# Kernel tuning notes

Measured on AMD Instinct MI355X. Metric: run time of the kernel, lower is better.

The kernel has to match this reference:

```python
import jax, jax.numpy as jnp
import numpy as np
import math

V, D, H, F, L, S, B = 50257, 1024, 16, 4096, 4, 2048, 2
DK = D // H

def setup_inputs() -> dict:
    key = jax.random.key(0)
    ks = iter(jax.random.split(key, 32))
    std = 0.02
    def nrm(shape):
        return (std * jax.random.normal(next(ks), shape)).astype(jnp.float32)
    inp = {
        "x": jax.random.randint(next(ks), (B, S), 0, V, dtype=jnp.int32),
        "emb": nrm((V, D)),
        "ln1_g": jnp.ones((L, D), jnp.float32), "ln1_b": jnp.zeros((L, D), jnp.float32),
        "wq": nrm((L, D, D)), "wk": nrm((L, D, D)), "wv": nrm((L, D, D)), "wo": nrm((L, D, D)),
        "ln2_g": jnp.ones((L, D), jnp.float32), "ln2_b": jnp.zeros((L, D), jnp.float32),
        "w1": nrm((L, D, F)), "b1": jnp.zeros((L, F), jnp.float32),
        "w2": nrm((L, F, D)), "b2": jnp.zeros((L, D), jnp.float32),
        "lnf_g": jnp.ones((D,), jnp.float32), "lnf_b": jnp.zeros((D,), jnp.float32),
        "head_w": nrm((D, V)), "head_b": jnp.zeros((V,), jnp.float32),
    }
    return inp

def _layernorm(x, g, b, eps=1e-5):
    mu = jnp.mean(x, axis=-1, keepdims=True)
    var = jnp.var(x, axis=-1, keepdims=True)
    return (x - mu) * jax.lax.rsqrt(var + eps) * g + b

def _posenc(seq_len, d_model, dtype):
    pos = jnp.arange(seq_len, dtype=jnp.float32)[:, None]                  # [S,1]
    div = jnp.exp(jnp.arange(0, d_model, 2, dtype=jnp.float32) * (-math.log(10000.0) / d_model))
    ang = pos * div                                                        # [S,D/2]
    pe = jnp.stack([jnp.sin(ang), jnp.cos(ang)], axis=-1).reshape(seq_len, d_model)
    return pe.astype(dtype)

def reference(x, emb, ln1_g, ln1_b, wq, wk, wv, wo, ln2_g, ln2_b, w1, b1, w2, b2, lnf_g, lnf_b, head_w, head_b):
    b, s = x.shape
    h = emb[x] + _posenc(s, D, emb.dtype)[None]                            # [B,S,D]
    causal = jnp.tril(jnp.ones((s, s), dtype=bool))                       # True = keep
    scale = 1.0 / math.sqrt(DK)
    neg_inf = jnp.finfo(h.dtype).min
    for l in range(L):
        # --- attention sublayer ---
        hn = _layernorm(h, ln1_g[l], ln1_b[l])
        q = (hn @ wq[l]).reshape(b, s, H, DK)
        k = (hn @ wk[l]).reshape(b, s, H, DK)
        v = (hn @ wv[l]).reshape(b, s, H, DK)
        scores = jnp.einsum("bqhd,bkhd->bhqk", q, k) * scale
        scores = jnp.where(causal[None, None], scores, neg_inf)
        w = jax.nn.softmax(scores, axis=-1)
        attn = jnp.einsum("bhqk,bkhd->bqhd", w, v).reshape(b, s, D)
        h = h + attn @ wo[l]
        # --- FFN sublayer ---
        hn = _layernorm(h, ln2_g[l], ln2_b[l])
        h = h + jax.nn.relu(hn @ w1[l] + b1[l]) @ w2[l] + b2[l]
    h = _layernorm(h, lnf_g, lnf_b)
    logits = h @ head_w + head_b                                           # [B,S,V]
    return logits
```

## Files before the change

### kernel.cpp

```cpp
#include <hip/hip_runtime.h>
#include <math.h>

#define VOCAB 50257
#define VPAD  50432
#define DM    1024
#define NH    16
#define DKH   64
#define FF    4096
#define NL    4
#define SEQ   2048
#define BATCH 2
#define MROWS (BATCH*SEQ)

typedef __bf16 bf16_t;
typedef __bf16 bf16x8 __attribute__((ext_vector_type(8)));
typedef __bf16 bf16x4 __attribute__((ext_vector_type(4)));
typedef float  f32x4  __attribute__((ext_vector_type(4)));

typedef void as1_void __attribute__((address_space(1)));
typedef void as3_void __attribute__((address_space(3)));

__device__ __forceinline__ void gload_lds16(const void* g, void* l) {
  __builtin_amdgcn_global_load_lds((as1_void*)g, (as3_void*)l, 16, 0, 0);
}

__device__ __forceinline__ uint32_t lds_addr32(const void* p) {
  return (uint32_t)(uintptr_t)(as3_void*)p;
}

__device__ __forceinline__ bf16x8 dsr128(uint32_t addr) {
  bf16x8 v;
  asm volatile("ds_read_b128 %0, %1" : "=v"(v) : "v"(addr));
  return v;
}

#define FENCE asm volatile("" ::: "memory")
#define BAR() do { FENCE; __builtin_amdgcn_s_barrier(); FENCE; } while (0)
#define LGKM0_FENCE() do { \
  asm volatile("s_waitcnt lgkmcnt(0)" ::: "memory"); \
  __builtin_amdgcn_sched_barrier(0); \
} while (0)

__global__ __launch_bounds__(256) void embed_kernel(const int* __restrict__ x,
    const float* __restrict__ emb, float* __restrict__ h) {
  int row = blockIdx.x;
  int s = row & (SEQ - 1);
  int d = threadIdx.x * 4;
  const float* e = emb + (size_t)x[row] * DM + d;
  float4 v = *(const float4*)e;
  float vin[4] = {v.x, v.y, v.z, v.w};
  float out[4];
#pragma unroll
  for (int j = 0; j < 4; ++j) {
    int dd = d + j;
    int i = dd >> 1;
    float freq = expf(-0.017988946039016376f * (float)i);
    float ang = (float)s * freq;
    float pe = (dd & 1) ? cosf(ang) : sinf(ang);
    out[j] = vin[j] + pe;
  }
  *(float4*)(h + (size_t)row * DM + d) = make_float4(out[0], out[1], out[2], out[3]);
}

__global__ __launch_bounds__(256) void ln_kernel(const float* __restrict__ x,
    const float* __restrict__ g, const float* __restrict__ b, bf16_t* __restrict__ out) {
  int row = blockIdx.x;
  int tid = threadIdx.x, lane = tid & 63, wave = tid >> 6;
  const float* xr = x + (size_t)row * DM;
  float4 v = ((const float4*)xr)[tid];
  float s1 = v.x + v.y + v.z + v.w;
  float s2 = v.x * v.x + v.y * v.y + v.z * v.z + v.w * v.w;
#pragma unroll
  for (int d = 1; d < 64; d <<= 1) { s1 += __shfl_xor(s1, d); s2 += __shfl_xor(s2, d); }
  __shared__ float red[8];
  if (lane == 0) { red[wave] = s1; red[4 + wave] = s2; }
  __syncthreads();
  s1 = red[0] + red[1] + red[2] + red[3];
  s2 = red[4] + red[5] + red[6] + red[7];
  float mu = s1 * (1.0f / DM);
  float var = s2 * (1.0f / DM) - mu * mu;
  float rs = rsqrtf(var + 1e-5f);
  float4 gv = ((const float4*)g)[tid];
  float4 bv = ((const float4*)b)[tid];
  bf16x4 o;
  o[0] = (bf16_t)((v.x - mu) * rs * gv.x + bv.x);
  o[1] = (bf16_t)((v.y - mu) * rs * gv.y + bv.y);
  o[2] = (bf16_t)((v.z - mu) * rs * gv.z + bv.z);
  o[3] = (bf16_t)((v.w - mu) * rs * gv.w + bv.w);
  *(bf16x4*)(out + (size_t)row * DM + tid * 4) = o;
}

__global__ __launch_bounds__(256) void transpose_cast_kernel(const float* __restrict__ in,
    bf16_t* __restrict__ out, int K, int N, int Npad) {
  __shared__ float tile[32][33];
  int n0 = blockIdx.x * 32, k0 = blockIdx.y * 32;
  int tx = threadIdx.x & 31, ty = threadIdx.x >> 5;
#pragma unroll
  for (int kk = ty; kk < 32; kk += 8) {
    int n = n0 + tx;
    tile[kk][tx] = (n < N) ? in[(size_t)(k0 + kk) * N + n] : 0.f;
  }
  __syncthreads();
#pragma unroll
  for (int nn = ty; nn < 32; nn += 8) {
    out[(size_t)(n0 + nn) * K + k0 + tx] = (bf16_t)tile[tx][nn];
  }
}

__global__ __launch_bounds__(256) void qkvtrans_kernel(const float* __restrict__ wq,
    const float* __restrict__ wk, const float* __restrict__ wv, bf16_t* __restrict__ out) {
  __shared__ float tile[32][33];
  int z = blockIdx.z;
  const float* in = (z == 0) ? wq : (z == 1) ? wk : wv;
  bf16_t* dst = out + (size_t)z * DM * DM;
  int n0 = blockIdx.x * 32, k0 = blockIdx.y * 32;
  int tx = threadIdx.x & 31, ty = threadIdx.x >> 5;
#pragma unroll
  for (int kk = ty; kk < 32; kk += 8)
    tile[kk][tx] = in[(size_t)(k0 + kk) * DM + n0 + tx];
  __syncthreads();
#pragma unroll
  for (int nn = ty; nn < 32; nn += 8)
    dst[(size_t)(n0 + nn) * DM + k0 + tx] = (bf16_t)tile[tx][nn];
}

__global__ __launch_bounds__(256) void vtrans_kernel(const bf16_t* __restrict__ qkv,
    bf16_t* __restrict__ vT) {
  int sb = blockIdx.x, hh = blockIdx.y, bb = blockIdx.z;
  __shared__ bf16_t t[64][72];
  int tid = threadIdx.x;
  const bf16_t* src = qkv + ((size_t)bb * SEQ + sb * 64) * (3 * DM) + 2 * DM + hh * DKH;
#pragma unroll
  for (int c = 0; c < 2; ++c) {
    int u = c * 256 + tid;
    int s = u >> 3, d8 = u & 7;
    *(bf16x8*)&t[s][d8 * 8] = *(const bf16x8*)(src + (size_t)s * (3 * DM) + d8 * 8);
  }
  __syncthreads();
  bf16_t* dst = vT + ((size_t)(bb * NH + hh) * DKH) * SEQ + sb * 64;
#pragma unroll
  for (int c = 0; c < 2; ++c) {
    int u = c * 256 + tid;
    int dk = u >> 3, s8 = u & 7;
    bf16x8 v;
#pragma unroll
    for (int j = 0; j < 8; ++j) v[j] = t[s8 * 8 + j][dk];
    *(bf16x8*)(dst + (size_t)dk * SEQ + s8 * 8) = v;
  }
}

__global__ __launch_bounds__(256, 2) void gemm128_kernel(
    const bf16_t* __restrict__ A, const bf16_t* __restrict__ Bt, int K,
    const float* __restrict__ bias, const float* __restrict__ Rsd,
    float* Cf, bf16_t* Cb, int ldc, int Nvalid, int relu, int gridM, int gridN) {
  __shared__ __align__(16) bf16_t lds[32768];

  int nwg = gridM * gridN;
  int orig = blockIdx.x;
  int q = nwg >> 3, rr = nwg & 7;
  int xcd = orig & 7, idx = orig >> 3;
  int swz = (xcd < rr ? xcd * (q + 1) : rr * (q + 1) + (xcd - rr) * q) + idx;
  int bm = swz % gridM, bn = swz / gridM;
  int m0 = bm * 128, n0 = bn * 128;

  int tid = threadIdx.x, lane = tid & 63, wave = tid >> 6;
  int g = lane >> 4, r = lane & 15;
  int wr = wave >> 1, wc = wave & 1;

  f32x4 zero = {0.f, 0.f, 0.f, 0.f};
  f32x4 acc[4][4];
#pragma unroll
  for (int i = 0; i < 4; ++i)
#pragma unroll
    for (int j = 0; j < 4; ++j) acc[i][j] = zero;

  const bf16_t* Abase = A + (size_t)m0 * K;
  const bf16_t* Bbase = Bt + (size_t)n0 * K;
  int NT = K >> 6;

  uint32_t L0 = lds_addr32(lds);
  uint32_t aF = L0 + (uint32_t)((g * 128 + wr * 64 + r) * 16);
  uint32_t bF = L0 + 32768u + (uint32_t)((g * 128 + wc * 64 + r) * 16);

  auto stage = [&](int t) {
    int b = t & 1, k0 = t << 6;
    bf16_t* dA = lds + (size_t)b * 8192;
    bf16_t* dB = lds + 16384 + (size_t)b * 8192;
#pragma unroll
    for (int j = 0; j < 4; ++j) {
      int u = j * 256 + tid;
      int row = u & 127, k8 = u >> 7;
      gload_lds16(Abase + (size_t)row * K + k0 + k8 * 8, dA + (j * 256 + wave * 64) * 8);
    }
#pragma unroll
    for (int j = 0; j < 4; ++j) {
      int u = j * 256 + tid;
      int row = u & 127, k8 = u >> 7;
      gload_lds16(Bbase + (size_t)row * K + k0 + k8 * 8, dB + (j * 256 + wave * 64) * 8);
    }
  };

  stage(0);
  if (NT > 1) {
    stage(1);
    asm volatile("s_waitcnt vmcnt(8)" ::: "memory");
  } else {
    asm volatile("s_waitcnt vmcnt(0)" ::: "memory");
  }
  BAR();

  for (int t = 0; t < NT; ++t) {
    uint32_t boff = (uint32_t)((t & 1) << 14);
    bf16x8 af[4][2], bfr[4][2];
#pragma unroll
    for (int mr = 0; mr < 4; ++mr)
#pragma unroll
      for (int kk = 0; kk < 2; ++kk)
        af[mr][kk] = dsr128(aF + boff + (uint32_t)(kk * 8192 + mr * 256));
#pragma unroll
    for (int nr = 0; nr < 4; ++nr)
#pragma unroll
      for (int kk = 0; kk < 2; ++kk)
        bfr[nr][kk] = dsr128(bF + boff + (uint32_t)(kk * 8192 + nr * 256));
    LGKM0_FENCE();
    BAR();
    if (t + 2 < NT) stage(t + 2);
    __builtin_amdgcn_s_setprio(1);
#pragma unroll
    for (int mr = 0; mr < 4; ++mr)
#pragma unroll
      for (int nr = 0; nr < 4; ++nr) {
        acc[mr][nr] = __builtin_amdgcn_mfma_f32_16x16x32_bf16(af[mr][0], bfr[nr][0], acc[mr][nr], 0, 0, 0);
        acc[mr][nr] = __builtin_amdgcn_mfma_f32_16x16x32_bf16(af[mr][1], bfr[nr][1], acc[mr][nr], 0, 0, 0);
      }
    __builtin_amdgcn_s_setprio(0);
    __builtin_amdgcn_sched_barrier(0);
    if (t + 2 < NT) {
      asm volatile("s_waitcnt vmcnt(8)" ::: "memory");
    } else {
      asm volatile("s_waitcnt vmcnt(0)" ::: "memory");
    }
    BAR();
  }

#pragma unroll
  for (int mr = 0; mr < 4; ++mr) {
    int row = m0 + wr * 64 + mr * 16 + g * 4;
#pragma unroll
    for (int nr = 0; nr < 4; ++nr) {
      int col = n0 + wc * 64 + nr * 16 + r;
      if (col < Nvalid) {
        float bval = bias ? bias[col] : 0.f;
#pragma unroll
        for (int i = 0; i < 4; ++i) {
          float vv = acc[mr][nr][i] + bval;
          if (relu) vv = fmaxf(vv, 0.f);
          size_t idxo = (size_t)(row + i) * ldc + col;
          if (Rsd) vv += Rsd[idxo];
          if (Cf) Cf[idxo] = vv;
          if (Cb) Cb[idxo] = (bf16_t)vv;
        }
      }
    }
  }
}

__global__ __launch_bounds__(512, 2) void gemm256_kernel(
    const bf16_t* __restrict__ A, const bf16_t* __restrict__ Bt, int K,
    const float* __restrict__ bias, float* Cf, bf16_t* Cb,
    int ldc, int Nvalid, int relu, int gridM, int gridN) {
  __shared__ __align__(16) bf16_t lds[65536];

  int nwg = gridM * gridN;
  int orig = blockIdx.x;
  int q = nwg >> 3, rr = nwg & 7;
  int xcd = orig & 7, idx = orig >> 3;
  int swz = (xcd < rr ? xcd * (q + 1) : rr * (q + 1) + (xcd - rr) * q) + idx;
  int bm = swz % gridM, bn = swz / gridM;
  int m0 = bm * 256, n0 = bn * 256;

  int tid = threadIdx.x, lane = tid & 63, wave = tid >> 6;
  int g = lane >> 4, r = lane & 15;
  int wr = wave >> 2, wc = wave & 3;

  f32x4 zero = {0.f, 0.f, 0.f, 0.f};
  f32x4 acc[8][4];
#pragma unroll
  for (int i = 0; i < 8; ++i)
#pragma unroll
    for (int j = 0; j < 4; ++j) acc[i][j] = zero;

  const bf16_t* Ab = A + (size_t)m0 * K;
  const bf16_t* Bb = Bt + (size_t)n0 * K;
  int NT = K >> 6;

  uint32_t L0 = lds_addr32(lds);
  uint32_t laneOff = (uint32_t)(g * 2048 + r * 16);
  uint32_t aBase0 = L0 + ((uint32_t)wr << 14) + laneOff;
  uint32_t bBase0 = L0 + 65536u + ((uint32_t)(wc >> 1) << 14) + laneOff
                  + (uint32_t)((wc & 1) * 1024);

  auto stageA = [&](int t, int hh) {
    int b = t & 1, k0 = t << 6;
    const bf16_t* src = Ab + (size_t)(hh * 128) * K + k0;
    bf16_t* dst = lds + (size_t)(b * 2 + hh) * 8192;
#pragma unroll
    for (int j = 0; j < 2; ++j) {
      int u = j * 512 + tid;
      gload_lds16(src + (size_t)(u & 127) * K + (u >> 7) * 8, dst + (j * 512 + wave * 64) * 8);
    }
  };
  auto stageB = [&](int t, int hh) {
    int b = t & 1, k0 = t << 6;
    const bf16_t* src = Bb + (size_t)(hh * 128) * K + k0;
    bf16_t* dst = lds + 32768 + (size_t)(b * 2 + hh) * 8192;
#pragma unroll
    for (int j = 0; j < 2; ++j) {
      int u = j * 512 + tid;
      gload_lds16(src + (size_t)(u & 127) * K + (u >> 7) * 8, dst + (j * 512 + wave * 64) * 8);
    }
  };

  stageB(0, 0); stageB(0, 1); stageA(0, 0); stageA(0, 1);
  if (NT > 1) {
    stageB(1, 0); stageB(1, 1);
    asm volatile("s_waitcnt vmcnt(4)" ::: "memory");
  } else {
    asm volatile("s_waitcnt vmcnt(0)" ::: "memory");
  }
  BAR();

  for (int t = 0; t < NT; ++t) {
    uint32_t bsel = (uint32_t)((t & 1) << 15);
    uint32_t Aaddr = aBase0 + bsel;
    uint32_t Baddr = bBase0 + bsel;

    bf16x8 a0[4][2], a1[4][2], b01[2][2], b23[2][2];

#pragma unroll
    for (int mi = 0; mi < 4; ++mi)
#pragma unroll
      for (int kk = 0; kk < 2; ++kk)
        a0[mi][kk] = dsr128(Aaddr + (uint32_t)(kk * 8192 + mi * 256));
#pragma unroll
    for (int ni = 0; ni < 2; ++ni)
#pragma unroll
      for (int kk = 0; kk < 2; ++kk)
        b01[ni][kk] = dsr128(Baddr + (uint32_t)(kk * 8192 + ni * 256));
    if (t + 1 < NT) stageA(t + 1, 0);
    BAR();
    LGKM0_FENCE();
    __builtin_amdgcn_s_setprio(1);
#pragma unroll
    for (int mi = 0; mi < 4; ++mi)
#pragma unroll
      for (int ni = 0; ni < 2; ++ni)
#pragma unroll
        for (int kk = 0; kk < 2; ++kk)
          acc[mi][ni] = __builtin_amdgcn_mfma_f32_16x16x32_bf16(a0[mi][kk], b01[ni][kk], acc[mi][ni], 0, 0, 0);
    __builtin_amdgcn_s_setprio(0);
    __builtin_amdgcn_sched_barrier(0);
    BAR();

#pragma unroll
    for (int ni = 0; ni < 2; ++ni)
#pragma unroll
      for (int kk = 0; kk < 2; ++kk)
        b23[ni][kk] = dsr128(Baddr + (uint32_t)(kk * 8192 + (ni + 2) * 256));
    if (t + 1 < NT) stageA(t + 1, 1);
    BAR();
    LGKM0_FENCE();
    __builtin_amdgcn_s_setprio(1);
#pragma unroll
    for (int mi = 0; mi < 4; ++mi)
#pragma unroll
      for (int ni = 0; ni < 2; ++ni)
#pragma unroll
        for (int kk = 0; kk < 2; ++kk)
          acc[mi][ni + 2] = __builtin_amdgcn_mfma_f32_16x16x32_bf16(a0[mi][kk], b23[ni][kk], acc[mi][ni + 2], 0, 0, 0);
    __builtin_amdgcn_s_setprio(0);
    __builtin_amdgcn_sched_barrier(0);
    BAR();

#pragma unroll
    for (int mi = 0; mi < 4; ++mi)
#pragma unroll
      for (int kk = 0; kk < 2; ++kk)
        a1[mi][kk] = dsr128(Aaddr + (uint32_t)(kk * 8192 + (mi + 4) * 256));
    if (t + 2 < NT) stageB(t + 2, 0);
    BAR();
    LGKM0_FENCE();
    __builtin_amdgcn_s_setprio(1);
#pragma unroll
    for (int mi = 0; mi < 4; ++mi)
#pragma unroll
      for (int ni = 0; ni < 2; ++ni)
#pragma unroll
        for (int kk = 0; kk < 2; ++kk)
          acc[mi + 4][ni] = __builtin_amdgcn_mfma_f32_16x16x32_bf16(a1[mi][kk], b01[ni][kk], acc[mi + 4][ni], 0, 0, 0);
    __builtin_amdgcn_s_setprio(0);
    __builtin_amdgcn_sched_barrier(0);
    BAR();

    if (t + 2 < NT) stageB(t + 2, 1);
    __builtin_amdgcn_sched_barrier(0);
    __builtin_amdgcn_s_setprio(1);
#pragma unroll
    for (int mi = 0; mi < 4; ++mi)
#pragma unroll
      for (int ni = 0; ni < 2; ++ni)
#pragma unroll
        for (int kk = 0; kk < 2; ++kk)
          acc[mi + 4][ni + 2] = __builtin_amdgcn_mfma_f32_16x16x32_bf16(a1[mi][kk], b23[ni][kk], acc[mi + 4][ni + 2], 0, 0, 0);
    __builtin_amdgcn_s_setprio(0);
    __builtin_amdgcn_sched_barrier(0);
    if (t + 2 < NT) {
      asm volatile("s_waitcnt vmcnt(4)" ::: "memory");
    } else {
      asm volatile("s_waitcnt vmcnt(0)" ::: "memory");
    }
    BAR();
  }

#pragma unroll
  for (int mi = 0; mi < 8; ++mi) {
    int row = m0 + wr * 128 + mi * 16 + g * 4;
#pragma unroll
    for (int ni = 0; ni < 4; ++ni) {
      int col = n0 + wc * 64 + ni * 16 + r;
      if (col < Nvalid) {
        float bval = bias ? bias[col] : 0.f;
#pragma unroll
        for (int i = 0; i < 4; ++i) {
          float vv = acc[mi][ni][i] + bval;
          if (relu) vv = fmaxf(vv, 0.f);
          size_t idxo = (size_t)(row + i) * ldc + col;
          if (Cf) Cf[idxo] = vv;
          if (Cb) Cb[idxo] = (bf16_t)vv;
        }
      }
    }
  }
}

__global__ __launch_bounds__(512, 4) void attn_kernel(const bf16_t* __restrict__ Qg,
    const bf16_t* __restrict__ Kg, const bf16_t* __restrict__ vT, bf16_t* __restrict__ Og,
    int ldq) {
  int bq = (int)gridDim.x - 1 - (int)blockIdx.x;
  int hh = blockIdx.y, bb = blockIdx.z;
  int tid = threadIdx.x, lane = tid & 63, wave = tid >> 6;
  int g = lane >> 4, r = lane & 15;
  __shared__ __align__(16) bf16_t Kl[4096];
  __shared__ __align__(16) bf16_t Vl[4096];
  __shared__ __align__(16) bf16_t Pl[8][1024];

  size_t base = (size_t)bb * SEQ * ldq + hh * DKH;
  size_t vbase = ((size_t)(bb * NH + hh)) * DKH * SEQ;
  size_t baseO = (size_t)bb * SEQ * DM + hh * DKH;
  int q0 = bq * 128 + wave * 16;
  const bf16_t* qrowp = Qg + base + (size_t)(q0 + r) * ldq;
  bf16x8 qf0 = *(const bf16x8*)(qrowp + g * 8);
  bf16x8 qf1 = *(const bf16x8*)(qrowp + 32 + g * 8);

  f32x4 zero = {0.f, 0.f, 0.f, 0.f};
  f32x4 accO[4];
#pragma unroll
  for (int dt = 0; dt < 4; ++dt) accO[dt] = zero;
  float m_i[4], l_i[4];
#pragma unroll
  for (int i = 0; i < 4; ++i) { m_i[i] = -1e30f; l_i[i] = 0.f; }
  const float scale = 0.125f;

  int skv = tid >> 3, kslot = tid & 7, kdk8 = kslot ^ (skv & 7);
  int sdk = tid >> 3, vslot = tid & 7, vkv8 = vslot ^ (sdk & 7);
  const bf16_t* ksrc0 = Kg + base + (size_t)skv * ldq + kdk8 * 8;
  const bf16_t* vsrc0 = vT + vbase + (size_t)sdk * SEQ + vkv8 * 8;

  int nkb = 2 * bq + 2;
  for (int kb = 0; kb < nkb; ++kb) {
    __syncthreads();
    gload_lds16(ksrc0 + (size_t)(kb * 64) * ldq, &Kl[(wave * 64) * 8]);
    gload_lds16(vsrc0 + kb * 64, &Vl[(wave * 64) * 8]);
    __syncthreads();

    f32x4 sc[4];
#pragma unroll
    for (int ct = 0; ct < 4; ++ct) {
      int kvrow = ct * 16 + r;
      bf16x8 kf0 = *(const bf16x8*)&Kl[(kvrow * 8 + (g ^ (r & 7))) * 8];
      bf16x8 kf1 = *(const bf16x8*)&Kl[(kvrow * 8 + ((4 + g) ^ (r & 7))) * 8];
      f32x4 s = zero;
      s = __builtin_amdgcn_mfma_f32_16x16x32_bf16(qf0, kf0, s, 0, 0, 0);
      s = __builtin_amdgcn_mfma_f32_16x16x32_bf16(qf1, kf1, s, 0, 0, 0);
      sc[ct] = s;
    }

#pragma unroll
    for (int i = 0; i < 4; ++i) {
      int qglob = q0 + g * 4 + i;
      float mx = m_i[i];
#pragma unroll
      for (int ct = 0; ct < 4; ++ct) {
        int kglob = kb * 64 + ct * 16 + r;
        float s = sc[ct][i] * scale;
        s = (kglob <= qglob) ? s : -1e30f;
        sc[ct][i] = s;
        mx = fmaxf(mx, s);
      }
#pragma unroll
      for (int d = 1; d < 16; d <<= 1) mx = fmaxf(mx, __shfl_xor(mx, d));
      float scl = __expf(m_i[i] - mx);
      l_i[i] *= scl;
      m_i[i] = mx;
      float rsum = 0.f;
#pragma unroll
      for (int ct = 0; ct < 4; ++ct) {
        float p = __expf(sc[ct][i] - mx);
        sc[ct][i] = p;
        rsum += p;
      }
#pragma unroll
      for (int d = 1; d < 16; d <<= 1) rsum += __shfl_xor(rsum, d);
      l_i[i] += rsum;
#pragma unroll
      for (int dt = 0; dt < 4; ++dt) accO[dt][i] *= scl;
    }

#pragma unroll
    for (int ct = 0; ct < 4; ++ct) {
      int kcol = ct * 16 + r;
#pragma unroll
      for (int i = 0; i < 4; ++i)
        Pl[wave][((kcol >> 3) * 16 + g * 4 + i) * 8 + (kcol & 7)] = (bf16_t)sc[ct][i];
    }

    bf16x8 pa0 = *(const bf16x8*)&Pl[wave][((0 + g) * 16 + r) * 8];
    bf16x8 pa1 = *(const bf16x8*)&Pl[wave][((4 + g) * 16 + r) * 8];
#pragma unroll
    for (int dt = 0; dt < 4; ++dt) {
      int dkrow = dt * 16 + r;
      bf16x8 vb0 = *(const bf16x8*)&Vl[(dkrow * 8 + (g ^ (r & 7))) * 8];
      bf16x8 vb1 = *(const bf16x8*)&Vl[(dkrow * 8 + ((4 + g) ^ (r & 7))) * 8];
      accO[dt] = __builtin_amdgcn_mfma_f32_16x16x32_bf16(pa0, vb0, accO[dt], 0, 0, 0);
      accO[dt] = __builtin_amdgcn_mfma_f32_16x16x32_bf16(pa1, vb1, accO[dt], 0, 0, 0);
    }
  }

#pragma unroll
  for (int dt = 0; dt < 4; ++dt)
#pragma unroll
    for (int i = 0; i < 4; ++i) {
      int rowq = q0 + g * 4 + i;
      Og[baseO + (size_t)rowq * DM + dt * 16 + r] = (bf16_t)(accO[dt][i] / l_i[i]);
    }
}

static inline void launch_gemm256(const bf16_t* A, const bf16_t* Bt, int K,
    const float* bias, float* Cf, bf16_t* Cb, int ldc, int Nvalid, int relu,
    int M, int Npad, hipStream_t stream) {
  int gridM = M / 256, gridN = Npad / 256;
  gemm256_kernel<<<dim3(gridM * gridN), 512, 0, stream>>>(
      A, Bt, K, bias, Cf, Cb, ldc, Nvalid, relu, gridM, gridN);
}

static inline void launch_gemm128(const bf16_t* A, const bf16_t* Bt, int K,
    const float* bias, const float* Rsd, float* Cf, bf16_t* Cb,
    int ldc, int Nvalid, int relu, int M, int Npad, hipStream_t stream) {
  int gridM = M / 128, gridN = Npad / 128;
  gemm128_kernel<<<dim3(gridM * gridN), 256, 0, stream>>>(
      A, Bt, K, bias, Rsd, Cf, Cb, ldc, Nvalid, relu, gridM, gridN);
}

extern "C" void kernel_launch(void* const* d_in, const int* in_sizes, int n_in,
                              void* d_out, int out_size, void* d_ws, size_t ws_size,
                              hipStream_t stream) {
  const int*   x      = (const int*)d_in[0];
  const float* emb    = (const float*)d_in[1];
  const float* ln1_g  = (const float*)d_in[2];
  const float* ln1_b  = (const float*)d_in[3];
  const float* wq     = (const float*)d_in[4];
  const float* wk     = (const float*)d_in[5];
  const float* wv     = (const float*)d_in[6];
  const float* wo     = (const float*)d_in[7];
  const float* ln2_g  = (const float*)d_in[8];
  const float* ln2_b  = (const float*)d_in[9];
  const float* w1     = (const float*)d_in[10];
  const float* b1     = (const float*)d_in[11];
  const float* w2     = (const float*)d_in[12];
  const float* b2     = (const float*)d_in[13];
  const float* lnf_g  = (const float*)d_in[14];
  const float* lnf_b  = (const float*)d_in[15];
  const float* head_w = (const float*)d_in[16];
  const float* head_b = (const float*)d_in[17];
  float* out = (float*)d_out;

  char* ws = (char*)d_ws;
  size_t off = 0;
  auto alloc = [&](size_t bytes) -> void* {
    void* p = ws + off;
    off += (bytes + 255) & ~(size_t)255;
    return p;
  };
  float*  h     = (float*)alloc((size_t)MROWS * DM * 4);
  bf16_t* hn    = (bf16_t*)alloc((size_t)MROWS * DM * 2);
  bf16_t* qkv   = (bf16_t*)alloc((size_t)MROWS * 3 * DM * 2);
  bf16_t* atb   = (bf16_t*)alloc((size_t)MROWS * DM * 2);
  bf16_t* ffn1  = (bf16_t*)alloc((size_t)MROWS * FF * 2);
  bf16_t* vTb   = (bf16_t*)alloc((size_t)BATCH * NH * DKH * SEQ * 2);
  bf16_t* headT = (bf16_t*)alloc((size_t)VPAD * DM * 2);
  bf16_t* wqkvT = headT;
  bf16_t* wT    = headT + (size_t)4 * DM * DM;

  embed_kernel<<<MROWS, 256, 0, stream>>>(x, emb, h);

  for (int l = 0; l < NL; ++l) {
    ln_kernel<<<MROWS, 256, 0, stream>>>(h, ln1_g + l * DM, ln1_b + l * DM, hn);

    qkvtrans_kernel<<<dim3(DM / 32, DM / 32, 3), 256, 0, stream>>>(
        wq + (size_t)l * DM * DM, wk + (size_t)l * DM * DM, wv + (size_t)l * DM * DM, wqkvT);
    launch_gemm256(hn, wqkvT, DM, nullptr, nullptr, qkv, 3 * DM, 3 * DM, 0,
                   MROWS, 3 * DM, stream);

    vtrans_kernel<<<dim3(SEQ / 64, NH, BATCH), 256, 0, stream>>>(qkv, vTb);
    attn_kernel<<<dim3(SEQ / 128, NH, BATCH), 512, 0, stream>>>(
        qkv, qkv + DM, vTb, atb, 3 * DM);

    transpose_cast_kernel<<<dim3(DM / 32, DM / 32), 256, 0, stream>>>(
        wo + (size_t)l * DM * DM, wT, DM, DM, DM);
    launch_gemm128(atb, wT, DM, nullptr, h, h, nullptr, DM, DM, 0, MROWS, DM, stream);

    ln_kernel<<<MROWS, 256, 0, stream>>>(h, ln2_g + l * DM, ln2_b + l * DM, hn);

    transpose_cast_kernel<<<dim3(FF / 32, DM / 32), 256, 0, stream>>>(
        w1 + (size_t)l * DM * FF, wT, DM, FF, FF);
    launch_gemm256(hn, wT, DM, b1 + (size_t)l * FF, nullptr, ffn1, FF, FF, 1,
                   MROWS, FF, stream);

    transpose_cast_kernel<<<dim3(DM / 32, FF / 32), 256, 0, stream>>>(
        w2 + (size_t)l * FF * DM, wT, FF, DM, DM);
    launch_gemm128(ffn1, wT, FF, b2 + (size_t)l * DM, h, h, nullptr, DM, DM, 0,
                   MROWS, DM, stream);
  }

  ln_kernel<<<MROWS, 256, 0, stream>>>(h, lnf_g, lnf_b, hn);
  transpose_cast_kernel<<<dim3(VPAD / 32, DM / 32), 256, 0, stream>>>(
      head_w, headT, DM, VOCAB, VPAD);
  launch_gemm128(hn, headT, DM, head_b, nullptr, out, nullptr, VOCAB, VOCAB, 0,
                 MROWS, VPAD, stream);
}
```

Measured before the change: 2.696 ms.

## Double-buffer attention K/V tiles, merge per-layer weight transposes, use 256 GEMM for head

The attention kernel now double-buffers K/V tiles in LDS with async global-to-LDS loads, so the fetch of the next tile overlaps compute. It also folds the softmax scale into Q, skips causal masking on fully visible blocks, and batches LDS reads before the MFMAs. The per-layer weight transposes for wq/wk/wv/wo/w1/w2 are merged into one launch. The vocab head projection switches from the 128 GEMM to the 256-tile GEMM. Pre-scaling Q in bf16 adds a small rounding change, and the double-buffered K/V doubles the K/V LDS footprint, which may reduce occupancy.

Result: faster. 2.260 ms (-16.2%).

```diff
diff --git a/kernel.cpp b/kernel.cpp
--- a/kernel.cpp
+++ b/kernel.cpp
@@ -107,21 +107,38 @@
   }
 }
 
-__global__ __launch_bounds__(256) void qkvtrans_kernel(const float* __restrict__ wq,
-    const float* __restrict__ wk, const float* __restrict__ wv, bf16_t* __restrict__ out) {
+__global__ __launch_bounds__(256) void wtrans_kernel(
+    const float* __restrict__ wq, const float* __restrict__ wk,
+    const float* __restrict__ wv, const float* __restrict__ wo,
+    const float* __restrict__ w1, const float* __restrict__ w2,
+    bf16_t* __restrict__ qkvT, bf16_t* __restrict__ woT,
+    bf16_t* __restrict__ w1T, bf16_t* __restrict__ w2T) {
+  int id = blockIdx.x;
+  const float* src; bf16_t* dst; int K, N, tk, tn;
+  if (id < 4096) {
+    int m = id >> 10, tile_i = id & 1023;
+    tk = tile_i >> 5; tn = tile_i & 31; K = 1024; N = 1024;
+    src = (m == 0) ? wq : (m == 1) ? wk : (m == 2) ? wv : wo;
+    dst = (m < 3) ? qkvT + (size_t)m * DM * DM : woT;
+  } else if (id < 8192) {
+    int tile_i = id - 4096;
+    tk = tile_i >> 7; tn = tile_i & 127; K = 1024; N = 4096;
+    src = w1; dst = w1T;
+  } else {
+    int tile_i = id - 8192;
+    tk = tile_i >> 5; tn = tile_i & 31; K = 4096; N = 1024;
+    src = w2; dst = w2T;
+  }
   __shared__ float tile[32][33];
-  int z = blockIdx.z;
-  const float* in = (z == 0) ? wq : (z == 1) ? wk : wv;
-  bf16_t* dst = out + (size_t)z * DM * DM;
-  int n0 = blockIdx.x * 32, k0 = blockIdx.y * 32;
+  int n0 = tn * 32, k0 = tk * 32;
   int tx = threadIdx.x & 31, ty = threadIdx.x >> 5;
 #pragma unroll
   for (int kk = ty; kk < 32; kk += 8)
-    tile[kk][tx] = in[(size_t)(k0 + kk) * DM + n0 + tx];
+    tile[kk][tx] = src[(size_t)(k0 + kk) * N + n0 + tx];
   __syncthreads();
 #pragma unroll
   for (int nn = ty; nn < 32; nn += 8)
-    dst[(size_t)(n0 + nn) * DM + k0 + tx] = (bf16_t)tile[tx][nn];
+    dst[(size_t)(n0 + nn) * K + k0 + tx] = (bf16_t)tile[tx][nn];
 }
 
 __global__ __launch_bounds__(256) void vtrans_kernel(const bf16_t* __restrict__ qkv,
@@ -450,8 +467,8 @@
   int hh = blockIdx.y, bb = blockIdx.z;
   int tid = threadIdx.x, lane = tid & 63, wave = tid >> 6;
   int g = lane >> 4, r = lane & 15;
-  __shared__ __align__(16) bf16_t Kl[4096];
-  __shared__ __align__(16) bf16_t Vl[4096];
+  __shared__ __align__(16) bf16_t Kl[2][4096];
+  __shared__ __align__(16) bf16_t Vl[2][4096];
   __shared__ __align__(16) bf16_t Pl[8][1024];
 
   size_t base = (size_t)bb * SEQ * ldq + hh * DKH;
@@ -461,6 +478,15 @@
   const bf16_t* qrowp = Qg + base + (size_t)(q0 + r) * ldq;
   bf16x8 qf0 = *(const bf16x8*)(qrowp + g * 8);
   bf16x8 qf1 = *(const bf16x8*)(qrowp + 32 + g * 8);
+#pragma unroll
+  for (int j = 0; j < 8; ++j) {
+    qf0[j] = (bf16_t)((float)qf0[j] * 0.125f);
+    qf1[j] = (bf16_t)((float)qf1[j] * 0.125f);
+  }
+
+  uint32_t KlA = lds_addr32(&Kl[0][0]);
+  uint32_t VlA = lds_addr32(&Vl[0][0]);
+  int slot0 = g ^ (r & 7), slot1 = (4 + g) ^ (r & 7);
 
   f32x4 zero = {0.f, 0.f, 0.f, 0.f};
   f32x4 accO[4];
@@ -469,43 +495,60 @@
   float m_i[4], l_i[4];
 #pragma unroll
   for (int i = 0; i < 4; ++i) { m_i[i] = -1e30f; l_i[i] = 0.f; }
-  const float scale = 0.125f;
 
   int skv = tid >> 3, kslot = tid & 7, kdk8 = kslot ^ (skv & 7);
   int sdk = tid >> 3, vslot = tid & 7, vkv8 = vslot ^ (sdk & 7);
   const bf16_t* ksrc0 = Kg + base + (size_t)skv * ldq + kdk8 * 8;
   const bf16_t* vsrc0 = vT + vbase + (size_t)sdk * SEQ + vkv8 * 8;
 
+  auto stage = [&](int kb) {
+    int c = kb & 1;
+    gload_lds16(ksrc0 + (size_t)(kb * 64) * ldq, &Kl[c][(wave * 64) * 8]);
+    gload_lds16(vsrc0 + kb * 64, &Vl[c][(wave * 64) * 8]);
+  };
+
   int nkb = 2 * bq + 2;
+  stage(0); stage(1);
+  asm volatile("s_waitcnt vmcnt(2)" ::: "memory");
+  BAR();
+
   for (int kb = 0; kb < nkb; ++kb) {
-    __syncthreads();
-    gload_lds16(ksrc0 + (size_t)(kb * 64) * ldq, &Kl[(wave * 64) * 8]);
-    gload_lds16(vsrc0 + kb * 64, &Vl[(wave * 64) * 8]);
-    __syncthreads();
-
-    f32x4 sc[4];
+    uint32_t koff = KlA + (uint32_t)((kb & 1) << 13);
+    uint32_t voff = VlA + (uint32_t)((kb & 1) << 13);
+
+    bf16x8 kf[4][2];
 #pragma unroll
     for (int ct = 0; ct < 4; ++ct) {
       int kvrow = ct * 16 + r;
-      bf16x8 kf0 = *(const bf16x8*)&Kl[(kvrow * 8 + (g ^ (r & 7))) * 8];
-      bf16x8 kf1 = *(const bf16x8*)&Kl[(kvrow * 8 + ((4 + g) ^ (r & 7))) * 8];
+      kf[ct][0] = dsr128(koff + (uint32_t)((kvrow * 8 + slot0) * 16));
+      kf[ct][1] = dsr128(koff + (uint32_t)((kvrow * 8 + slot1) * 16));
+    }
+    LGKM0_FENCE();
+    f32x4 sc[4];
+#pragma unroll
+    for (int ct = 0; ct < 4; ++ct) {
       f32x4 s = zero;
-      s = __builtin_amdgcn_mfma_f32_16x16x32_bf16(qf0, kf0, s, 0, 0, 0);
-      s = __builtin_amdgcn_mfma_f32_16x16x32_bf16(qf1, kf1, s, 0, 0, 0);
+      s = __builtin_amdgcn_mfma_f32_16x16x32_bf16(qf0, kf[ct][0], s, 0, 0, 0);
+      s = __builtin_amdgcn_mfma_f32_16x16x32_bf16(qf1, kf[ct][1], s, 0, 0, 0);
       sc[ct] = s;
     }
 
+    bool full = (kb * 64 + 63) <= q0;
 #pragma unroll
     for (int i = 0; i < 4; ++i) {
-      int qglob = q0 + g * 4 + i;
       float mx = m_i[i];
-#pragma unroll
-      for (int ct = 0; ct < 4; ++ct) {
-        int kglob = kb * 64 + ct * 16 + r;
-        float s = sc[ct][i] * scale;
-        s = (kglob <= qglob) ? s : -1e30f;
-        sc[ct][i] = s;
-        mx = fmaxf(mx, s);
+      if (full) {
+#pragma unroll
+        for (int ct = 0; ct < 4; ++ct) mx = fmaxf(mx, sc[ct][i]);
+      } else {
+        int qglob = q0 + g * 4 + i;
+#pragma unroll
+        for (int ct = 0; ct < 4; ++ct) {
+          int kglob = kb * 64 + ct * 16 + r;
+          float s = (kglob <= qglob) ? sc[ct][i] : -1e30f;
+          sc[ct][i] = s;
+          mx = fmaxf(mx, s);
+        }
       }
 #pragma unroll
       for (int d = 1; d < 16; d <<= 1) mx = fmaxf(mx, __shfl_xor(mx, d));
@@ -533,17 +576,31 @@
       for (int i = 0; i < 4; ++i)
         Pl[wave][((kcol >> 3) * 16 + g * 4 + i) * 8 + (kcol & 7)] = (bf16_t)sc[ct][i];
     }
-
     bf16x8 pa0 = *(const bf16x8*)&Pl[wave][((0 + g) * 16 + r) * 8];
     bf16x8 pa1 = *(const bf16x8*)&Pl[wave][((4 + g) * 16 + r) * 8];
+
+    bf16x8 vb[4][2];
 #pragma unroll
     for (int dt = 0; dt < 4; ++dt) {
       int dkrow = dt * 16 + r;
-      bf16x8 vb0 = *(const bf16x8*)&Vl[(dkrow * 8 + (g ^ (r & 7))) * 8];
-      bf16x8 vb1 = *(const bf16x8*)&Vl[(dkrow * 8 + ((4 + g) ^ (r & 7))) * 8];
-      accO[dt] = __builtin_amdgcn_mfma_f32_16x16x32_bf16(pa0, vb0, accO[dt], 0, 0, 0);
-      accO[dt] = __builtin_amdgcn_mfma_f32_16x16x32_bf16(pa1, vb1, accO[dt], 0, 0, 0);
-    }
+      vb[dt][0] = dsr128(voff + (uint32_t)((dkrow * 8 + slot0) * 16));
+      vb[dt][1] = dsr128(voff + (uint32_t)((dkrow * 8 + slot1) * 16));
+    }
+    LGKM0_FENCE();
+#pragma unroll
+    for (int dt = 0; dt < 4; ++dt) {
+      accO[dt] = __builtin_amdgcn_mfma_f32_16x16x32_bf16(pa0, vb[dt][0], accO[dt], 0, 0, 0);
+      accO[dt] = __builtin_amdgcn_mfma_f32_16x16x32_bf16(pa1, vb[dt][1], accO[dt], 0, 0, 0);
+    }
+
+    BAR();
+    if (kb + 2 < nkb) {
+      stage(kb + 2);
+      asm volatile("s_waitcnt vmcnt(2)" ::: "memory");
+    } else {
+      asm volatile("s_waitcnt vmcnt(0)" ::: "memory");
+    }
+    BAR();
   }
 
 #pragma unroll
@@ -609,15 +666,20 @@
   bf16_t* vTb   = (bf16_t*)alloc((size_t)BATCH * NH * DKH * SEQ * 2);
   bf16_t* headT = (bf16_t*)alloc((size_t)VPAD * DM * 2);
   bf16_t* wqkvT = headT;
-  bf16_t* wT    = headT + (size_t)4 * DM * DM;
+  bf16_t* woT   = headT + (size_t)3 * DM * DM;
+  bf16_t* w1T   = headT + (size_t)4 * DM * DM;
+  bf16_t* w2T   = headT + (size_t)4 * DM * DM + (size_t)DM * FF;
 
   embed_kernel<<<MROWS, 256, 0, stream>>>(x, emb, h);
 
   for (int l = 0; l < NL; ++l) {
     ln_kernel<<<MROWS, 256, 0, stream>>>(h, ln1_g + l * DM, ln1_b + l * DM, hn);
 
-    qkvtrans_kernel<<<dim3(DM / 32, DM / 32, 3), 256, 0, stream>>>(
-        wq + (size_t)l * DM * DM, wk + (size_t)l * DM * DM, wv + (size_t)l * DM * DM, wqkvT);
+    wtrans_kernel<<<12288, 256, 0, stream>>>(
+        wq + (size_t)l * DM * DM, wk + (size_t)l * DM * DM, wv + (size_t)l * DM * DM,
+        wo + (size_t)l * DM * DM, w1 + (size_t)l * DM * FF, w2 + (size_t)l * FF * DM,
+        wqkvT, woT, w1T, w2T);
+
     launch_gemm256(hn, wqkvT, DM, nullptr, nullptr, qkv, 3 * DM, 3 * DM, 0,
                    MROWS, 3 * DM, stream);
 
@@ -625,26 +687,20 @@
     attn_kernel<<<dim3(SEQ / 128, NH, BATCH), 512, 0, stream>>>(
         qkv, qkv + DM, vTb, atb, 3 * DM);
 
-    transpose_cast_kernel<<<dim3(DM / 32, DM / 32), 256, 0, stream>>>(
-        wo + (size_t)l * DM * DM, wT, DM, DM, DM);
-    launch_gemm128(atb, wT, DM, nullptr, h, h, nullptr, DM, DM, 0, MROWS, DM, stream);
+    launch_gemm128(atb, woT, DM, nullptr, h, h, nullptr, DM, DM, 0, MROWS, DM, stream);
 
     ln_kernel<<<MROWS, 256, 0, stream>>>(h, ln2_g + l * DM, ln2_b + l * DM, hn);
 
-    transpose_cast_kernel<<<dim3(FF / 32, DM / 32), 256, 0, stream>>>(
-        w1 + (size_t)l * DM * FF, wT, DM, FF, FF);
-    launch_gemm256(hn, wT, DM, b1 + (size_t)l * FF, nullptr, ffn1, FF, FF, 1,
+    launch_gemm256(hn, w1T, DM, b1 + (size_t)l * FF, nullptr, ffn1, FF, FF, 1,
                    MROWS, FF, stream);
 
-    transpose_cast_kernel<<<dim3(DM / 32, FF / 32), 256, 0, stream>>>(
-        w2 + (size_t)l * FF * DM, wT, FF, DM, DM);
-    launch_gemm128(ffn1, wT, FF, b2 + (size_t)l * DM, h, h, nullptr, DM, DM, 0,
+    launch_gemm128(ffn1, w2T, FF, b2 + (size_t)l * DM, h, h, nullptr, DM, DM, 0,
                    MROWS, DM, stream);
   }
 
   ln_kernel<<<MROWS, 256, 0, stream>>>(h, lnf_g, lnf_b, hn);
   transpose_cast_kernel<<<dim3(VPAD / 32, DM / 32), 256, 0, stream>>>(
       head_w, headT, DM, VOCAB, VPAD);
-  launch_gemm128(hn, headT, DM, head_b, nullptr, out, nullptr, VOCAB, VOCAB, 0,
+  launch_gemm256(hn, headT, DM, head_b, out, nullptr, VOCAB, VOCAB, 0,
                  MROWS, VPAD, stream);
 }
```
